# Kernel optimization log

Measured on AMD Instinct MI355X. Metric: run time of the kernel, lower is better.

Reference implementation:

```python
import jax, jax.numpy as jnp
import numpy as np

FEATURE_NUM = 27  # 1 dense + 26 sparse features


def setup_inputs() -> dict:
    key = jax.random.key(0)
    k1, k2 = jax.random.split(key)
    B, N, D = 65536, FEATURE_NUM - 1, 128
    dense_features = jax.random.normal(k1, (B, D), dtype=jnp.float32)
    sparse_features = jax.random.normal(k2, (B, N, D), dtype=jnp.float32)
    return {"dense_features": dense_features, "sparse_features": sparse_features}


def reference(dense_features, sparse_features):
    # combined: (B, F, D) with F = feature_num = 1 + N
    combined = jnp.concatenate([dense_features[:, None, :], sparse_features], axis=1)
    # full Gram matrix (B, F, F), matching the original bmm
    interactions = jnp.einsum("bfd,bgd->bfg", combined, combined)
    # strictly-upper-triangular gather (row-major i<j), same order as torch.triu_indices
    iu, ju = jnp.triu_indices(FEATURE_NUM, k=1)
    return interactions[:, iu, ju]  # (B, F*(F-1)/2)
```

## Files before the change

### kernel.cpp

```cpp
#include <hip/hip_runtime.h>


constexpr int F      = 27;
constexpr int NPAIRS = F * (F - 1) / 2;
constexpr int D      = 128;
constexpr int DC     = 32;
constexpr int NQ     = DC / 4;
constexpr int SPB    = 8;
constexpr int RP     = 36;
constexpr int LPS    = F * RP;
constexpr int NT     = 7;
constexpr int NTP    = NT * (NT + 1) / 2;

__global__ __launch_bounds__(256)
void interact_kernel(const float* __restrict__ dense,
                     const float* __restrict__ sparse,
                     float* __restrict__ out, int B) {
    __shared__ float lds[SPB * LPS];

    const int tid = threadIdx.x;
    const int s   = tid >> 5;
    const int p   = tid & 31;
    const long b  = (long)blockIdx.x * SPB + s;

    int ti = 0, rem = p;
    while (ti < NT - 1 && rem >= NT - ti) { rem -= NT - ti; ++ti; }
    int tj = ti + rem;

    float acc[4][4];
    #pragma unroll
    for (int a = 0; a < 4; ++a)
        #pragma unroll
        for (int c = 0; c < 4; ++c) acc[a][c] = 0.0f;

    const int nload = SPB * F * NQ;

    for (int c = 0; c < D / DC; ++c) {
        __syncthreads();
        for (int idx = tid; idx < nload; idx += 256) {
            int q  = idx & (NQ - 1);
            int t  = idx >> 3;
            int ls = t / F;
            int n  = t - ls * F;
            long bb = (long)blockIdx.x * SPB + ls;
            if (bb < B) {
                const float* src = (n == 0)
                    ? dense  + bb * (long)D + c * DC + q * 4
                    : sparse + ((bb * 26) + (n - 1)) * (long)D + c * DC + q * 4;
                float4 v = *(const float4*)src;
                *(float4*)&lds[(ls * F + n) * RP + q * 4] = v;
            }
        }
        __syncthreads();
        const float* base = &lds[s * LPS];
        #pragma unroll
        for (int dq = 0; dq < DC; dq += 4) {
            float4 av[4], bv[4];
            #pragma unroll
            for (int a = 0; a < 4; ++a) {
                int ri = ti + 7 * a; ri = ri < F ? ri : F - 1;
                int rj = tj + 7 * a; rj = rj < F ? rj : F - 1;
                av[a] = *(const float4*)&base[ri * RP + dq];
                bv[a] = *(const float4*)&base[rj * RP + dq];
            }
            #pragma unroll
            for (int a = 0; a < 4; ++a)
                #pragma unroll
                for (int bq = 0; bq < 4; ++bq) {
                    acc[a][bq] = fmaf(av[a].x, bv[bq].x, acc[a][bq]);
                    acc[a][bq] = fmaf(av[a].y, bv[bq].y, acc[a][bq]);
                    acc[a][bq] = fmaf(av[a].z, bv[bq].z, acc[a][bq]);
                    acc[a][bq] = fmaf(av[a].w, bv[bq].w, acc[a][bq]);
                }
        }
    }

    if (p < NTP && b < B) {
        float* ob = out + b * (long)NPAIRS;
        #pragma unroll
        for (int a = 0; a < 4; ++a) {
            int ri = ti + 7 * a;
            if (ri >= F) continue;
            #pragma unroll
            for (int bq = 0; bq < 4; ++bq) {
                int rj = tj + 7 * bq;
                if (rj >= F) continue;
                if (ti == tj) {
                    if (a >= bq) continue;
                }
                int i = ri < rj ? ri : rj;
                int j = ri < rj ? rj : ri;
                int o = i * (2 * F - i - 1) / 2 + (j - i - 1);
                ob[o] = acc[a][bq];
            }
        }
    }
}

extern "C" void kernel_launch(void* const* d_in, const int* in_sizes, int n_in,
                              void* d_out, int out_size, void* d_ws, size_t ws_size,
                              hipStream_t stream) {
    const float* dense  = (const float*)d_in[0];
    const float* sparse = (const float*)d_in[1];
    float* out = (float*)d_out;
    const int B = in_sizes[0] / D;
    const int grid = (B + SPB - 1) / SPB;
    interact_kernel<<<grid, 256, 0, stream>>>(dense, sparse, out, B);
}
```

Measured before the change: 1.185 ms.

## Compute Gram matrix with bf16x3 split MFMA per wavefront, removing LDS staging

Replaces the LDS-tiled FP32 FMA kernel with one wavefront per sample that loads its 27 rows straight into registers. Each value is split into bf16 hi/lo parts, and three 32x32x16 bf16 MFMAs per K-step emulate FP32 accuracy. This drops the shared-memory staging, the block barriers and the scalar FMA work, so the kernel should be bound by memory bandwidth. In exchange, precision falls slightly below true FP32 since the lo*lo term is omitted, and the 32x32 tile wastes 5 rows on padding.

```diff
diff --git a/kernel.cpp b/kernel.cpp
--- a/kernel.cpp
+++ b/kernel.cpp
@@ -4,95 +4,77 @@
 constexpr int F      = 27;
 constexpr int NPAIRS = F * (F - 1) / 2;
 constexpr int D      = 128;
-constexpr int DC     = 32;
-constexpr int NQ     = DC / 4;
-constexpr int SPB    = 8;
-constexpr int RP     = 36;
-constexpr int LPS    = F * RP;
-constexpr int NT     = 7;
-constexpr int NTP    = NT * (NT + 1) / 2;
+constexpr int SPB    = 4;
+
+typedef __attribute__((ext_vector_type(8)))  short bf16x8;
+typedef __attribute__((ext_vector_type(16))) float f32x16;
+
+__device__ __forceinline__ unsigned short f32_to_bf16_rne(float x) {
+    unsigned u = __float_as_uint(x);
+    unsigned r = u + 0x7fffu + ((u >> 16) & 1u);
+    return (unsigned short)(r >> 16);
+}
+__device__ __forceinline__ float bf16_to_f32(unsigned short h) {
+    return __uint_as_float((unsigned)h << 16);
+}
 
 __global__ __launch_bounds__(256)
-void interact_kernel(const float* __restrict__ dense,
-                     const float* __restrict__ sparse,
-                     float* __restrict__ out, int B) {
-    __shared__ float lds[SPB * LPS];
+void interact_mfma(const float* __restrict__ dense,
+                   const float* __restrict__ sparse,
+                   float* __restrict__ out, int B) {
+    const int tid = threadIdx.x;
+    const int l   = tid & 63;
+    const int r   = l & 31;
+    const int h   = l >> 5;
+    const long b  = (long)blockIdx.x * SPB + (tid >> 6);
+    if (b >= B) return;
 
-    const int tid = threadIdx.x;
-    const int s   = tid >> 5;
-    const int p   = tid & 31;
-    const long b  = (long)blockIdx.x * SPB + s;
+    const bool valid = (r < F);
+    const float* rowp = (r == 0 || !valid)
+        ? dense  + b * (long)D
+        : sparse + (b * 26L + (r - 1)) * (long)D;
 
-    int ti = 0, rem = p;
-    while (ti < NT - 1 && rem >= NT - ti) { rem -= NT - ti; ++ti; }
-    int tj = ti + rem;
-
-    float acc[4][4];
+    float4 v[16];
     #pragma unroll
-    for (int a = 0; a < 4; ++a)
-        #pragma unroll
-        for (int c = 0; c < 4; ++c) acc[a][c] = 0.0f;
-
-    const int nload = SPB * F * NQ;
-
-    for (int c = 0; c < D / DC; ++c) {
-        __syncthreads();
-        for (int idx = tid; idx < nload; idx += 256) {
-            int q  = idx & (NQ - 1);
-            int t  = idx >> 3;
-            int ls = t / F;
-            int n  = t - ls * F;
-            long bb = (long)blockIdx.x * SPB + ls;
-            if (bb < B) {
-                const float* src = (n == 0)
-                    ? dense  + bb * (long)D + c * DC + q * 4
-                    : sparse + ((bb * 26) + (n - 1)) * (long)D + c * DC + q * 4;
-                float4 v = *(const float4*)src;
-                *(float4*)&lds[(ls * F + n) * RP + q * 4] = v;
-            }
-        }
-        __syncthreads();
-        const float* base = &lds[s * LPS];
-        #pragma unroll
-        for (int dq = 0; dq < DC; dq += 4) {
-            float4 av[4], bv[4];
-            #pragma unroll
-            for (int a = 0; a < 4; ++a) {
-                int ri = ti + 7 * a; ri = ri < F ? ri : F - 1;
-                int rj = tj + 7 * a; rj = rj < F ? rj : F - 1;
-                av[a] = *(const float4*)&base[ri * RP + dq];
-                bv[a] = *(const float4*)&base[rj * RP + dq];
-            }
-            #pragma unroll
-            for (int a = 0; a < 4; ++a)
-                #pragma unroll
-                for (int bq = 0; bq < 4; ++bq) {
-                    acc[a][bq] = fmaf(av[a].x, bv[bq].x, acc[a][bq]);
-                    acc[a][bq] = fmaf(av[a].y, bv[bq].y, acc[a][bq]);
-                    acc[a][bq] = fmaf(av[a].z, bv[bq].z, acc[a][bq]);
-                    acc[a][bq] = fmaf(av[a].w, bv[bq].w, acc[a][bq]);
-                }
-        }
+    for (int t = 0; t < 8; ++t) {
+        const float* p = rowp + t * 16 + h * 8;
+        v[2 * t]     = *(const float4*)p;
+        v[2 * t + 1] = *(const float4*)(p + 4);
     }
 
-    if (p < NTP && b < B) {
-        float* ob = out + b * (long)NPAIRS;
+    f32x16 acc = {};
+
+    #pragma unroll
+    for (int t = 0; t < 8; ++t) {
+        float xs[8];
         #pragma unroll
-        for (int a = 0; a < 4; ++a) {
-            int ri = ti + 7 * a;
-            if (ri >= F) continue;
-            #pragma unroll
-            for (int bq = 0; bq < 4; ++bq) {
-                int rj = tj + 7 * bq;
-                if (rj >= F) continue;
-                if (ti == tj) {
-                    if (a >= bq) continue;
-                }
-                int i = ri < rj ? ri : rj;
-                int j = ri < rj ? rj : ri;
-                int o = i * (2 * F - i - 1) / 2 + (j - i - 1);
-                ob[o] = acc[a][bq];
-            }
+        for (int j = 0; j < 4; ++j) {
+            xs[j]     = (&v[2 * t].x)[j];
+            xs[j + 4] = (&v[2 * t + 1].x)[j];
+        }
+        bf16x8 hi, lo;
+        #pragma unroll
+        for (int j = 0; j < 8; ++j) {
+            float x = valid ? xs[j] : 0.0f;
+            unsigned short hb = f32_to_bf16_rne(x);
+            float lf = x - bf16_to_f32(hb);
+            hi[j] = (short)hb;
+            lo[j] = (short)f32_to_bf16_rne(lf);
+        }
+        acc = __builtin_amdgcn_mfma_f32_32x32x16_bf16(hi, hi, acc, 0, 0, 0);
+        acc = __builtin_amdgcn_mfma_f32_32x32x16_bf16(hi, lo, acc, 0, 0, 0);
+        acc = __builtin_amdgcn_mfma_f32_32x32x16_bf16(lo, hi, acc, 0, 0, 0);
+    }
+
+    if (!valid) return;
+    float* ob = out + b * (long)NPAIRS;
+    const int j = r;
+    #pragma unroll
+    for (int e = 0; e < 16; ++e) {
+        int i = (e & 3) + 8 * (e >> 2) + 4 * h;
+        if (i < j) {
+            int o = i * (2 * F - i - 1) / 2 + (j - i - 1);
+            ob[o] = acc[e];
         }
     }
 }
@@ -105,5 +87,5 @@
     float* out = (float*)d_out;
     const int B = in_sizes[0] / D;
     const int grid = (B + SPB - 1) / SPB;
-    interact_kernel<<<grid, 256, 0, stream>>>(dense, sparse, out, B);
+    interact_mfma<<<grid, 256, 0, stream>>>(dense, sparse, out, B);
 }
```

After: 1.161 ms. 1.02x faster.
